# Performance work log

Measured on AMD Instinct MI355X. Metric: run time of the kernel, lower is better.

## Reference

```python
import jax, jax.numpy as jnp
import numpy as np

N_NODES = 50000
N_EDGES = 800000
D = 128


def _graph_conv(x, W, b, src, dst, n_nodes):
    """DGL GraphConv with norm='both': D_in^{-1/2} A D_out^{-1/2} X W + b."""
    ones = jnp.ones((src.shape[0],), dtype=x.dtype)
    out_deg = jax.ops.segment_sum(ones, src, num_segments=n_nodes)
    in_deg = jax.ops.segment_sum(ones, dst, num_segments=n_nodes)
    out_norm = jax.lax.rsqrt(jnp.maximum(out_deg, 1.0))  # [N]
    in_norm = jax.lax.rsqrt(jnp.maximum(in_deg, 1.0))    # [N]
    # scale src features, transform (in_feats == out_feats so order is free), aggregate
    h = (x * out_norm[:, None]) @ W                       # [N, D]
    msgs = h[src]                                         # [E, D] gather
    agg = jax.ops.segment_sum(msgs, dst, num_segments=n_nodes)  # [N, D] scatter-add
    return agg * in_norm[:, None] + b


def setup_inputs() -> dict:
    key = jax.random.key(0)
    ks = jax.random.split(key, 8)
    x = jax.random.normal(ks[0], (N_NODES, D), dtype=jnp.float32)
    src = jax.random.randint(ks[1], (N_EDGES,), 0, N_NODES, dtype=jnp.int64)
    dst = jax.random.randint(ks[2], (N_EDGES,), 0, N_NODES, dtype=jnp.int64)
    scale = 1.0 / np.sqrt(D)
    W1 = jax.random.normal(ks[3], (D, D), dtype=jnp.float32) * scale
    W2 = jax.random.normal(ks[4], (D, D), dtype=jnp.float32) * scale
    W3 = jax.random.normal(ks[5], (D, D), dtype=jnp.float32) * scale
    b1 = jnp.zeros((D,), dtype=jnp.float32)
    b2 = jnp.zeros((D,), dtype=jnp.float32)
    b3 = jnp.zeros((D,), dtype=jnp.float32)
    return {"x": x, "src": src, "dst": dst,
            "W1": W1, "b1": b1, "W2": W2, "b2": b2, "W3": W3, "b3": b3}


def reference(x, src, dst, W1, b1, W2, b2, W3, b3):
    h = _graph_conv(x, W1, b1, src, dst, N_NODES)
    h = jax.nn.relu(h)
    h = _graph_conv(h, W2, b2, src, dst, N_NODES)
    h = jax.nn.relu(h)
    h = _graph_conv(h, W3, b3, src, dst, N_NODES)
    return h
```

## Files before the change

### kernel.cpp

```cpp
#include <hip/hip_runtime.h>
#include <hip/hip_fp16.h>

#define D 128
#define HB 128
#define HT 1024
#define WMAX 12800

struct alignas(16) H8 { __half2 h[4]; };
typedef _Float16 v8h __attribute__((ext_vector_type(8)));
typedef float v4f __attribute__((ext_vector_type(4)));


__global__ __launch_bounds__(HT) void hist_kernel(const int* __restrict__ src,
                                                  const int* __restrict__ dst,
                                                  unsigned* __restrict__ partial_out,
                                                  unsigned* __restrict__ partial_in,
                                                  unsigned char* __restrict__ lrank,
                                                  const float* __restrict__ W1,
                                                  const float* __restrict__ W2,
                                                  const float* __restrict__ W3,
                                                  _Float16* __restrict__ wt,
                                                  int nE, int W, int epb) {
    const int t = threadIdx.x;
    if ((int)blockIdx.x >= 2 * HB) {
        const int l = blockIdx.x - 2 * HB;
        const float* Wsrc = (l == 0) ? W1 : ((l == 1) ? W2 : W3);
        _Float16* o = wt + (size_t)l * D * D;
        for (int i = t; i < D * D; i += HT) {
            const int k = i >> 7, n = i & 127;
            o[n * D + k] = (_Float16)Wsrc[i];
        }
        return;
    }
    __shared__ unsigned lcnt[WMAX];
    const bool is_dst = (blockIdx.x < HB);
    const int b = is_dst ? blockIdx.x : (blockIdx.x - HB);
    for (int i = t; i < W; i += HT) lcnt[i] = 0;
    __syncthreads();
    const int e0 = b * epb;
    const int e1 = min(nE, e0 + epb);
    if (is_dst) {
        for (int e = e0 + t; e < e1; e += HT) {
            const int d = dst[e];
            const unsigned sh = (unsigned)(d & 3) * 8u;
            const unsigned old = atomicAdd(&lcnt[d >> 2], 1u << sh);
            lrank[e] = (unsigned char)((old >> sh) & 0xffu);
        }
    } else {
        for (int e = e0 + t; e < e1; e += HT) {
            const int s = src[e];
            atomicAdd(&lcnt[s >> 2], 1u << ((unsigned)(s & 3) * 8u));
        }
    }
    __syncthreads();
    unsigned* g = (is_dst ? partial_in : partial_out) + (size_t)b * W;
    for (int i = t; i < W; i += HT) g[i] = lcnt[i];
}

__global__ __launch_bounds__(256) void reduce_hist_kernel(const unsigned* __restrict__ partial_out,
                                                          const unsigned* __restrict__ partial_in,
                                                          unsigned* __restrict__ offs_in,
                                                          int* __restrict__ cnt_out,
                                                          int* __restrict__ cnt_in,
                                                          int W, int n, int nbW) {
    const bool is_dst = ((int)blockIdx.x < nbW);
    const int w = (is_dst ? blockIdx.x : (blockIdx.x - nbW)) * 256 + threadIdx.x;
    if (w >= W) return;
    unsigned run = 0;
    if (is_dst) {
#pragma unroll 16
        for (int b = 0; b < HB; ++b) {
            const unsigned c = partial_in[(size_t)b * W + w];
            offs_in[(size_t)b * W + w] = run;
            run += c;
        }
    } else {
#pragma unroll 16
        for (int b = 0; b < HB; ++b) run += partial_out[(size_t)b * W + w];
    }
    int* cnt = is_dst ? cnt_in : cnt_out;
    const int n0 = w * 4;
    const int4 c4 = make_int4((int)(run & 0xffu), (int)((run >> 8) & 0xffu),
                              (int)((run >> 16) & 0xffu), (int)((run >> 24) & 0xffu));
    if (n0 + 3 < n) {
        *(int4*)&cnt[n0] = c4;
    } else {
        const int* cp = &c4.x;
        for (int i = 0; i < 4 && n0 + i < n; ++i) cnt[n0 + i] = cp[i];
    }
}

__global__ __launch_bounds__(1024) void scan_block_kernel(const int* __restrict__ deg,
                                                          int* __restrict__ rp,
                                                          int* __restrict__ bsum, int n) {
    __shared__ int wsum[16];
    const int t = threadIdx.x;
    const int lane = t & 63;
    const int wid = t >> 6;
    const int i = blockIdx.x * 1024 + t;
    const int v = (i < n) ? deg[i] : 0;
    int s = v;
#pragma unroll
    for (int off = 1; off < 64; off <<= 1) {
        int u = __shfl_up(s, off, 64);
        if (lane >= off) s += u;
    }
    if (lane == 63) wsum[wid] = s;
    __syncthreads();
    if (wid == 0) {
        int ws = (lane < 16) ? wsum[lane] : 0;
#pragma unroll
        for (int off = 1; off < 16; off <<= 1) {
            int u = __shfl_up(ws, off, 64);
            if (lane >= off) ws += u;
        }
        if (lane < 16) wsum[lane] = ws;
    }
    __syncthreads();
    const int excl = s - v + ((wid > 0) ? wsum[wid - 1] : 0);
    if (i < n) rp[i] = excl;
    if (t == 0) bsum[blockIdx.x] = wsum[15];
}

__global__ __launch_bounds__(1024) void finalize_kernel(int* __restrict__ rp,
                                                        const int* __restrict__ bsum,
                                                        const int* __restrict__ cnt_out,
                                                        const int* __restrict__ cnt_in,
                                                        float* __restrict__ onorm,
                                                        float* __restrict__ inorm,
                                                        int n, int nb, int nE) {
    __shared__ int prefix_s;
    const int t = threadIdx.x;
    if (t < 64) {
        int v = (t < nb && t < (int)blockIdx.x) ? bsum[t] : 0;
#pragma unroll
        for (int off = 1; off < 64; off <<= 1) v += __shfl_xor(v, off, 64);
        if (t == 0) prefix_s = v;
    }
    __syncthreads();
    const int i = blockIdx.x * 1024 + t;
    if (i < n) {
        rp[i] += prefix_s;
        onorm[i] = rsqrtf(fmaxf((float)cnt_out[i], 1.0f));
        inorm[i] = rsqrtf(fmaxf((float)cnt_in[i], 1.0f));
    }
    if (blockIdx.x == 0 && t == 0) rp[n] = nE;
}

__global__ __launch_bounds__(1024) void gemm1_fill_kernel(
    const float* __restrict__ x, const _Float16* __restrict__ wt,
    const float* __restrict__ onorm, __half* __restrict__ y1, int nrows,
    const int* __restrict__ src, const int* __restrict__ dst,
    const unsigned char* __restrict__ lrank, const unsigned* __restrict__ offs_in,
    const int* __restrict__ rp, int* __restrict__ srcs_sorted,
    int nE, int epb, int W, int nGemmBlocks) {
    __shared__ _Float16 sA[128 * 136];
    __shared__ _Float16 sB[128 * 136];
    const int t = threadIdx.x;

    if ((int)blockIdx.x >= nGemmBlocks) {
        const int e = (blockIdx.x - nGemmBlocks) * 1024 + t;
        if (e < nE) {
            const int d = dst[e];
            const int b = e / epb;
            const unsigned off =
                (offs_in[(size_t)b * W + (d >> 2)] >> ((unsigned)(d & 3) * 8u)) & 0xffu;
            srcs_sorted[rp[d] + (int)off + (int)lrank[e]] = src[e];
        }
        return;
    }

    const int row0 = blockIdx.x * 128;
    const int rr = t >> 4;
    const int c8 = t & 15;
#pragma unroll
    for (int pass = 0; pass < 2; ++pass) {
        const int row = pass * 64 + rr;
        *(float4*)&sB[row * 136 + c8 * 8] = *(const float4*)&wt[(size_t)row * D + c8 * 8];
        const int grow = row0 + row;
        float4 u0 = make_float4(0.f, 0.f, 0.f, 0.f);
        float4 u1 = u0;
        if (grow < nrows) {
            const float* ap = x + (size_t)grow * D + c8 * 8;
            u0 = ((const float4*)ap)[0];
            u1 = ((const float4*)ap)[1];
        }
        v8h hv;
        hv[0] = (_Float16)u0.x; hv[1] = (_Float16)u0.y;
        hv[2] = (_Float16)u0.z; hv[3] = (_Float16)u0.w;
        hv[4] = (_Float16)u1.x; hv[5] = (_Float16)u1.y;
        hv[6] = (_Float16)u1.z; hv[7] = (_Float16)u1.w;
        *(v8h*)&sA[row * 136 + c8 * 8] = hv;
    }
    __syncthreads();

    const int w = t >> 6;
    const int lane = t & 63;
    const int m16 = lane & 15;
    const int quad = lane >> 4;
    const int rt = w >> 1;
    const int ch = w & 1;

    v4f c[4];
#pragma unroll
    for (int ct = 0; ct < 4; ++ct) c[ct] = (v4f){0.f, 0.f, 0.f, 0.f};

#pragma unroll
    for (int ks = 0; ks < 4; ++ks) {
        const v8h a = *(const v8h*)&sA[(rt * 16 + m16) * 136 + ks * 32 + quad * 8];
#pragma unroll
        for (int ct = 0; ct < 4; ++ct) {
            const v8h b = *(const v8h*)&sB[((ch * 4 + ct) * 16 + m16) * 136 + ks * 32 + quad * 8];
            c[ct] = __builtin_amdgcn_mfma_f32_16x16x32_f16(a, b, c[ct], 0, 0, 0);
        }
    }

#pragma unroll
    for (int r = 0; r < 4; ++r) {
        const int row = row0 + rt * 16 + quad * 4 + r;
        if (row < nrows) {
            const float osc = onorm[row];
#pragma unroll
            for (int ct = 0; ct < 4; ++ct) {
                const int col = (ch * 4 + ct) * 16 + m16;
                y1[(size_t)row * D + col] = __float2half(c[ct][r] * osc);
            }
        }
    }
}

template <bool EPI>
__global__ __launch_bounds__(256) void aggregate_kernel(const __half* __restrict__ xh,
                                                        const float* __restrict__ onorm,
                                                        const float* __restrict__ inorm,
                                                        const float* __restrict__ bias,
                                                        const int* __restrict__ rp,
                                                        const int* __restrict__ srcs,
                                                        __half* __restrict__ agg, int n_nodes) {
    const int node = blockIdx.x * 4 + (threadIdx.x >> 6);
    const int lane = threadIdx.x & 63;
    const int rg = lane >> 4;
    const int c8 = lane & 15;
    if (node >= n_nodes) return;
    const int e0 = rp[node];
    const int e1 = rp[node + 1];
    int e = e0 + rg;

    float acc[8];
#pragma unroll
    for (int j = 0; j < 8; ++j) acc[j] = 0.f;

    bool pr[8];
#pragma unroll
    for (int k = 0; k < 8; ++k) pr[k] = (e + 4 * k) < e1;
    int s[8];
#pragma unroll
    for (int k = 0; k < 8; ++k) {
        s[k] = 0;
        if (pr[k]) s[k] = __builtin_nontemporal_load(srcs + e + 4 * k);
    }
    H8 v[8];
#pragma unroll
    for (int k = 0; k < 8; ++k)
        v[k] = ((const H8*)(xh + (size_t)s[k] * D))[c8];
#pragma unroll
    for (int k = 0; k < 8; ++k) {
        if (pr[k]) {
#pragma unroll
            for (int j = 0; j < 4; ++j) {
                acc[2 * j]     = fmaf(__low2float(v[k].h[j]),  1.0f, acc[2 * j]);
                acc[2 * j + 1] = fmaf(__high2float(v[k].h[j]), 1.0f, acc[2 * j + 1]);
            }
        }
    }
    e += 32;

    while (__any(e < e1)) {
        bool q[4];
        int u[4];
#pragma unroll
        for (int k = 0; k < 4; ++k) {
            q[k] = (e + 4 * k) < e1;
            u[k] = 0;
            if (q[k]) u[k] = __builtin_nontemporal_load(srcs + e + 4 * k);
        }
        H8 w[4];
#pragma unroll
        for (int k = 0; k < 4; ++k)
            w[k] = ((const H8*)(xh + (size_t)u[k] * D))[c8];
#pragma unroll
        for (int k = 0; k < 4; ++k) {
            if (q[k]) {
#pragma unroll
                for (int j = 0; j < 4; ++j) {
                    acc[2 * j]     = fmaf(__low2float(w[k].h[j]),  1.0f, acc[2 * j]);
                    acc[2 * j + 1] = fmaf(__high2float(w[k].h[j]), 1.0f, acc[2 * j + 1]);
                }
            }
        }
        e += 16;
    }

    float r[8];
#pragma unroll
    for (int j = 0; j < 8; ++j) r[j] = acc[j];
#pragma unroll
    for (int off = 16; off < 64; off <<= 1)
#pragma unroll
        for (int j = 0; j < 8; ++j) r[j] += __shfl_xor(r[j], off, 64);

    if (rg == 0) {
        if (EPI) {
            const float inm = inorm[node];
            const float onm = onorm[node];
            const float4 bv0 = ((const float4*)bias)[c8 * 2];
            const float4 bv1 = ((const float4*)bias)[c8 * 2 + 1];
            const float* bp0 = &bv0.x;
            const float* bp1 = &bv1.x;
#pragma unroll
            for (int j = 0; j < 4; ++j) {
                r[j]     = fmaxf(fmaf(r[j],     inm, bp0[j]), 0.f) * onm;
                r[j + 4] = fmaxf(fmaf(r[j + 4], inm, bp1[j]), 0.f) * onm;
            }
        }
        H8 h;
#pragma unroll
        for (int j = 0; j < 4; ++j) h.h[j] = __floats2half2_rn(r[2 * j], r[2 * j + 1]);
        ((H8*)(agg + (size_t)node * D))[c8] = h;
    }
}

template <bool FULL, bool RELU, bool OSCALE, bool OUT16>
__global__ __launch_bounds__(256) void gemm_mfma_kernel(const __half* __restrict__ Ah,
                                                        const _Float16* __restrict__ Wt,
                                                        const float* __restrict__ bias,
                                                        const float* __restrict__ inorm,
                                                        const float* __restrict__ onorm,
                                                        void* __restrict__ outv, int nrows) {
    __shared__ _Float16 sA[128 * 136];
    __shared__ _Float16 sB[128 * 136];
    const int t = threadIdx.x;
    const int row0 = blockIdx.x * 128;
    const int rr = t >> 4;
    const int c8 = t & 15;

#pragma unroll
    for (int pass = 0; pass < 8; ++pass) {
        const int row = pass * 16 + rr;
        *(float4*)&sB[row * 136 + c8 * 8] = *(const float4*)&Wt[(size_t)row * D + c8 * 8];
        const int grow = row0 + row;
        float4 v = make_float4(0.f, 0.f, 0.f, 0.f);
        if (grow < nrows)
            v = *(const float4*)((const _Float16*)Ah + (size_t)grow * D + c8 * 8);
        *(float4*)&sA[row * 136 + c8 * 8] = v;
    }
    __syncthreads();

    const int w = t >> 6;
    const int lane = t & 63;
    const int m16 = lane & 15;
    const int quad = lane >> 4;

    v4f c[2][8];
#pragma unroll
    for (int rt = 0; rt < 2; ++rt)
#pragma unroll
        for (int ct = 0; ct < 8; ++ct) c[rt][ct] = (v4f){0.f, 0.f, 0.f, 0.f};

#pragma unroll
    for (int ks = 0; ks < 4; ++ks) {
        v8h afr[2], bfr[8];
#pragma unroll
        for (int rt = 0; rt < 2; ++rt)
            afr[rt] = *(const v8h*)&sA[(w * 32 + rt * 16 + m16) * 136 + ks * 32 + quad * 8];
#pragma unroll
        for (int ct = 0; ct < 8; ++ct)
            bfr[ct] = *(const v8h*)&sB[(ct * 16 + m16) * 136 + ks * 32 + quad * 8];
#pragma unroll
        for (int rt = 0; rt < 2; ++rt)
#pragma unroll
            for (int ct = 0; ct < 8; ++ct)
                c[rt][ct] = __builtin_amdgcn_mfma_f32_16x16x32_f16(afr[rt], bfr[ct], c[rt][ct], 0, 0, 0);
    }

#pragma unroll
    for (int rt = 0; rt < 2; ++rt) {
#pragma unroll
        for (int r = 0; r < 4; ++r) {
            const int row = row0 + w * 32 + rt * 16 + quad * 4 + r;
            if (row < nrows) {
                const float inm = FULL ? inorm[row] : 1.0f;
                const float osc = OSCALE ? onorm[row] : 1.0f;
#pragma unroll
                for (int ct = 0; ct < 8; ++ct) {
                    const int col = ct * 16 + m16;
                    float v = c[rt][ct][r];
                    if (FULL) v = fmaf(v, inm, bias[col]);
                    if (RELU) v = fmaxf(v, 0.f);
                    if (OSCALE) v *= osc;
                    if (OUT16) ((__half*)outv)[(size_t)row * D + col] = __float2half(v);
                    else       ((float*)outv)[(size_t)row * D + col] = v;
                }
            }
        }
    }
}

extern "C" void kernel_launch(void* const* d_in, const int* in_sizes, int n_in,
                              void* d_out, int out_size, void* d_ws, size_t ws_size,
                              hipStream_t stream) {
    const float* x   = (const float*)d_in[0];
    const int*   src = (const int*)d_in[1];
    const int*   dst = (const int*)d_in[2];
    const float* W1  = (const float*)d_in[3];
    const float* b1  = (const float*)d_in[4];
    const float* W2  = (const float*)d_in[5];
    const float* b2  = (const float*)d_in[6];
    const float* W3  = (const float*)d_in[7];
    const float* b3  = (const float*)d_in[8];

    const int N = in_sizes[0] / D;
    const int E = in_sizes[1];

    char* p = (char*)d_ws;
    auto alloc = [&](size_t bytes) -> void* {
        void* r = (void*)p;
        p += (bytes + 255) & ~(size_t)255;
        return r;
    };
    int*           cnt_out = (int*)alloc((size_t)N * 4);
    int*           cnt_in  = (int*)alloc((size_t)N * 4);
    int*           rp      = (int*)alloc((size_t)(N + 1) * 4);
    int*           bsum    = (int*)alloc(1024 * 4);
    float*         onorm   = (float*)alloc((size_t)N * 4);
    float*         inorm   = (float*)alloc((size_t)N * 4);
    int*           srcs    = (int*)alloc((size_t)E * 4);
    unsigned char* lrank   = (unsigned char*)alloc((size_t)E);
    _Float16*      wt      = (_Float16*)alloc((size_t)3 * D * D * 2);
    __half*        hbuf0   = (__half*)alloc((size_t)N * D * 2);
    __half*        hbuf1   = (__half*)alloc((size_t)N * D * 2);
    char*          scratch = (char*)alloc((size_t)3 * HB * ((N + 3) / 4) * 4);

    const int W = (N + 3) / 4;
    const int epb = (E + HB - 1) / HB;
    unsigned* partial_in  = (unsigned*)scratch;
    unsigned* partial_out = partial_in + (size_t)HB * W;
    unsigned* offs_in     = partial_out + (size_t)HB * W;
    __half*   abuf        = (__half*)scratch;
    float*    outf        = (float*)d_out;

    const int nb = (N + 1023) / 1024;
    const int nbW = (W + 255) / 256;
    const int gemmGrid = (N + 127) / 128;
    const int fillGrid = (E + 1023) / 1024;
    const int aggGrid = (N + 3) / 4;

    hist_kernel<<<2 * HB + 3, HT, 0, stream>>>(src, dst, partial_out, partial_in, lrank,
                                               W1, W2, W3, wt, E, W, epb);
    reduce_hist_kernel<<<2 * nbW, 256, 0, stream>>>(partial_out, partial_in, offs_in,
                                                    cnt_out, cnt_in, W, N, nbW);
    scan_block_kernel<<<nb, 1024, 0, stream>>>(cnt_in, rp, bsum, N);
    finalize_kernel<<<nb, 1024, 0, stream>>>(rp, bsum, cnt_out, cnt_in, onorm, inorm, N, nb, E);

    gemm1_fill_kernel<<<gemmGrid + fillGrid, 1024, 0, stream>>>(
        x, wt, onorm, hbuf0, N,
        src, dst, lrank, offs_in, rp, srcs, E, epb, W, gemmGrid);

    aggregate_kernel<true><<<aggGrid, 256, 0, stream>>>(
        hbuf0, onorm, inorm, b1, rp, srcs, hbuf1, N);
    aggregate_kernel<false><<<aggGrid, 256, 0, stream>>>(
        hbuf1, onorm, inorm, b2, rp, srcs, abuf, N);
    gemm_mfma_kernel<true, true, true, true><<<gemmGrid, 256, 0, stream>>>(
        abuf, wt + (size_t)D * D, b2, inorm, onorm, hbuf0, N);
    aggregate_kernel<false><<<aggGrid, 256, 0, stream>>>(
        hbuf0, onorm, inorm, b3, rp, srcs, abuf, N);
    gemm_mfma_kernel<true, false, false, false><<<gemmGrid, 256, 0, stream>>>(
        abuf, wt + (size_t)2 * D * D, b3, inorm, onorm, outf, N);
}
```

Before: 239.3 us.

## Fuse preprocessing kernels and move layer-one out-degree norm into per-edge weights

Merges the histogram, weight-transpose and first GEMM into one launch. The first GEMM no longer needs the out-degree norm, which is instead stored as a per-edge weight during the CSR fill and applied in the first aggregation. The scan is folded into the histogram reduction, and finalize is merged with the fill. The goal is fewer kernel launches and a shorter serial dependency chain before the first aggregation, at the cost of an extra per-edge float array read in the first aggregate and an uncoalesced W1 transpose load inside each GEMM block.

New measurement: 264.1 us. +10.4%, slower.

```diff
diff --git a/kernel.cpp b/kernel.cpp
--- a/kernel.cpp
+++ b/kernel.cpp
@@ -11,7 +11,7 @@
 typedef float v4f __attribute__((ext_vector_type(4)));
 
 
-__global__ __launch_bounds__(HT) void hist_kernel(const int* __restrict__ src,
+__global__ __launch_bounds__(HT) void mega_kernel(const int* __restrict__ src,
                                                   const int* __restrict__ dst,
                                                   unsigned* __restrict__ partial_out,
                                                   unsigned* __restrict__ partial_in,
@@ -20,11 +20,42 @@
                                                   const float* __restrict__ W2,
                                                   const float* __restrict__ W3,
                                                   _Float16* __restrict__ wt,
-                                                  int nE, int W, int epb) {
+                                                  const float* __restrict__ x,
+                                                  __half* __restrict__ y1,
+                                                  int nE, int W, int epb, int nrows) {
+    extern __shared__ char smem[];
     const int t = threadIdx.x;
-    if ((int)blockIdx.x >= 2 * HB) {
-        const int l = blockIdx.x - 2 * HB;
-        const float* Wsrc = (l == 0) ? W1 : ((l == 1) ? W2 : W3);
+
+    if ((int)blockIdx.x < 2 * HB) {
+        unsigned* lcnt = (unsigned*)smem;
+        const bool is_dst = (blockIdx.x < HB);
+        const int b = is_dst ? blockIdx.x : (blockIdx.x - HB);
+        for (int i = t; i < W; i += HT) lcnt[i] = 0;
+        __syncthreads();
+        const int e0 = b * epb;
+        const int e1 = min(nE, e0 + epb);
+        if (is_dst) {
+            for (int e = e0 + t; e < e1; e += HT) {
+                const int d = dst[e];
+                const unsigned sh = (unsigned)(d & 3) * 8u;
+                const unsigned old = atomicAdd(&lcnt[d >> 2], 1u << sh);
+                lrank[e] = (unsigned char)((old >> sh) & 0xffu);
+            }
+        } else {
+            for (int e = e0 + t; e < e1; e += HT) {
+                const int s = src[e];
+                atomicAdd(&lcnt[s >> 2], 1u << ((unsigned)(s & 3) * 8u));
+            }
+        }
+        __syncthreads();
+        unsigned* g = (is_dst ? partial_in : partial_out) + (size_t)b * W;
+        for (int i = t; i < W; i += HT) g[i] = lcnt[i];
+        return;
+    }
+
+    if ((int)blockIdx.x < 2 * HB + 2) {
+        const int l = blockIdx.x - 2 * HB + 1;
+        const float* Wsrc = (l == 1) ? W2 : W3;
         _Float16* o = wt + (size_t)l * D * D;
         for (int i = t; i < D * D; i += HT) {
             const int k = i >> 7, n = i & 127;
@@ -32,151 +63,19 @@
         }
         return;
     }
-    __shared__ unsigned lcnt[WMAX];
-    const bool is_dst = (blockIdx.x < HB);
-    const int b = is_dst ? blockIdx.x : (blockIdx.x - HB);
-    for (int i = t; i < W; i += HT) lcnt[i] = 0;
-    __syncthreads();
-    const int e0 = b * epb;
-    const int e1 = min(nE, e0 + epb);
-    if (is_dst) {
-        for (int e = e0 + t; e < e1; e += HT) {
-            const int d = dst[e];
-            const unsigned sh = (unsigned)(d & 3) * 8u;
-            const unsigned old = atomicAdd(&lcnt[d >> 2], 1u << sh);
-            lrank[e] = (unsigned char)((old >> sh) & 0xffu);
-        }
-    } else {
-        for (int e = e0 + t; e < e1; e += HT) {
-            const int s = src[e];
-            atomicAdd(&lcnt[s >> 2], 1u << ((unsigned)(s & 3) * 8u));
-        }
-    }
-    __syncthreads();
-    unsigned* g = (is_dst ? partial_in : partial_out) + (size_t)b * W;
-    for (int i = t; i < W; i += HT) g[i] = lcnt[i];
-}
-
-__global__ __launch_bounds__(256) void reduce_hist_kernel(const unsigned* __restrict__ partial_out,
-                                                          const unsigned* __restrict__ partial_in,
-                                                          unsigned* __restrict__ offs_in,
-                                                          int* __restrict__ cnt_out,
-                                                          int* __restrict__ cnt_in,
-                                                          int W, int n, int nbW) {
-    const bool is_dst = ((int)blockIdx.x < nbW);
-    const int w = (is_dst ? blockIdx.x : (blockIdx.x - nbW)) * 256 + threadIdx.x;
-    if (w >= W) return;
-    unsigned run = 0;
-    if (is_dst) {
-#pragma unroll 16
-        for (int b = 0; b < HB; ++b) {
-            const unsigned c = partial_in[(size_t)b * W + w];
-            offs_in[(size_t)b * W + w] = run;
-            run += c;
-        }
-    } else {
-#pragma unroll 16
-        for (int b = 0; b < HB; ++b) run += partial_out[(size_t)b * W + w];
-    }
-    int* cnt = is_dst ? cnt_in : cnt_out;
-    const int n0 = w * 4;
-    const int4 c4 = make_int4((int)(run & 0xffu), (int)((run >> 8) & 0xffu),
-                              (int)((run >> 16) & 0xffu), (int)((run >> 24) & 0xffu));
-    if (n0 + 3 < n) {
-        *(int4*)&cnt[n0] = c4;
-    } else {
-        const int* cp = &c4.x;
-        for (int i = 0; i < 4 && n0 + i < n; ++i) cnt[n0 + i] = cp[i];
-    }
-}
-
-__global__ __launch_bounds__(1024) void scan_block_kernel(const int* __restrict__ deg,
-                                                          int* __restrict__ rp,
-                                                          int* __restrict__ bsum, int n) {
-    __shared__ int wsum[16];
-    const int t = threadIdx.x;
-    const int lane = t & 63;
-    const int wid = t >> 6;
-    const int i = blockIdx.x * 1024 + t;
-    const int v = (i < n) ? deg[i] : 0;
-    int s = v;
-#pragma unroll
-    for (int off = 1; off < 64; off <<= 1) {
-        int u = __shfl_up(s, off, 64);
-        if (lane >= off) s += u;
-    }
-    if (lane == 63) wsum[wid] = s;
-    __syncthreads();
-    if (wid == 0) {
-        int ws = (lane < 16) ? wsum[lane] : 0;
-#pragma unroll
-        for (int off = 1; off < 16; off <<= 1) {
-            int u = __shfl_up(ws, off, 64);
-            if (lane >= off) ws += u;
-        }
-        if (lane < 16) wsum[lane] = ws;
-    }
-    __syncthreads();
-    const int excl = s - v + ((wid > 0) ? wsum[wid - 1] : 0);
-    if (i < n) rp[i] = excl;
-    if (t == 0) bsum[blockIdx.x] = wsum[15];
-}
-
-__global__ __launch_bounds__(1024) void finalize_kernel(int* __restrict__ rp,
-                                                        const int* __restrict__ bsum,
-                                                        const int* __restrict__ cnt_out,
-                                                        const int* __restrict__ cnt_in,
-                                                        float* __restrict__ onorm,
-                                                        float* __restrict__ inorm,
-                                                        int n, int nb, int nE) {
-    __shared__ int prefix_s;
-    const int t = threadIdx.x;
-    if (t < 64) {
-        int v = (t < nb && t < (int)blockIdx.x) ? bsum[t] : 0;
-#pragma unroll
-        for (int off = 1; off < 64; off <<= 1) v += __shfl_xor(v, off, 64);
-        if (t == 0) prefix_s = v;
-    }
-    __syncthreads();
-    const int i = blockIdx.x * 1024 + t;
-    if (i < n) {
-        rp[i] += prefix_s;
-        onorm[i] = rsqrtf(fmaxf((float)cnt_out[i], 1.0f));
-        inorm[i] = rsqrtf(fmaxf((float)cnt_in[i], 1.0f));
-    }
-    if (blockIdx.x == 0 && t == 0) rp[n] = nE;
-}
-
-__global__ __launch_bounds__(1024) void gemm1_fill_kernel(
-    const float* __restrict__ x, const _Float16* __restrict__ wt,
-    const float* __restrict__ onorm, __half* __restrict__ y1, int nrows,
-    const int* __restrict__ src, const int* __restrict__ dst,
-    const unsigned char* __restrict__ lrank, const unsigned* __restrict__ offs_in,
-    const int* __restrict__ rp, int* __restrict__ srcs_sorted,
-    int nE, int epb, int W, int nGemmBlocks) {
-    __shared__ _Float16 sA[128 * 136];
-    __shared__ _Float16 sB[128 * 136];
-    const int t = threadIdx.x;
-
-    if ((int)blockIdx.x >= nGemmBlocks) {
-        const int e = (blockIdx.x - nGemmBlocks) * 1024 + t;
-        if (e < nE) {
-            const int d = dst[e];
-            const int b = e / epb;
-            const unsigned off =
-                (offs_in[(size_t)b * W + (d >> 2)] >> ((unsigned)(d & 3) * 8u)) & 0xffu;
-            srcs_sorted[rp[d] + (int)off + (int)lrank[e]] = src[e];
-        }
-        return;
-    }
-
-    const int row0 = blockIdx.x * 128;
+
+    _Float16* sA = (_Float16*)smem;
+    _Float16* sB = sA + 128 * 136;
+    const int blk = blockIdx.x - (2 * HB + 2);
+    const int row0 = blk * 128;
     const int rr = t >> 4;
     const int c8 = t & 15;
 #pragma unroll
     for (int pass = 0; pass < 2; ++pass) {
         const int row = pass * 64 + rr;
-        *(float4*)&sB[row * 136 + c8 * 8] = *(const float4*)&wt[(size_t)row * D + c8 * 8];
+#pragma unroll
+        for (int j = 0; j < 8; ++j)
+            sB[row * 136 + c8 * 8 + j] = (_Float16)W1[(size_t)(c8 * 8 + j) * D + row];
         const int grow = row0 + row;
         float4 u0 = make_float4(0.f, 0.f, 0.f, 0.f);
         float4 u1 = u0;
@@ -219,23 +118,168 @@
     for (int r = 0; r < 4; ++r) {
         const int row = row0 + rt * 16 + quad * 4 + r;
         if (row < nrows) {
-            const float osc = onorm[row];
 #pragma unroll
             for (int ct = 0; ct < 4; ++ct) {
                 const int col = (ch * 4 + ct) * 16 + m16;
-                y1[(size_t)row * D + col] = __float2half(c[ct][r] * osc);
+                y1[(size_t)row * D + col] = __float2half(c[ct][r]);
             }
         }
     }
 }
 
-template <bool EPI>
+__global__ __launch_bounds__(256) void reduce_scan_kernel(const unsigned* __restrict__ partial_out,
+                                                          const unsigned* __restrict__ partial_in,
+                                                          unsigned* __restrict__ offs_in,
+                                                          int* __restrict__ cnt_out,
+                                                          int* __restrict__ cnt_in,
+                                                          int* __restrict__ rpp,
+                                                          int* __restrict__ bsum,
+                                                          int W, int n, int nbW) {
+    const int t = threadIdx.x;
+    if ((int)blockIdx.x >= nbW) {
+        const int w = (blockIdx.x - nbW) * 256 + t;
+        if (w >= W) return;
+        unsigned run = 0;
+#pragma unroll 16
+        for (int b = 0; b < HB; ++b) run += partial_out[(size_t)b * W + w];
+        const int n0 = w * 4;
+        const int4 c4 = make_int4((int)(run & 0xffu), (int)((run >> 8) & 0xffu),
+                                  (int)((run >> 16) & 0xffu), (int)((run >> 24) & 0xffu));
+        if (n0 + 3 < n) {
+            *(int4*)&cnt_out[n0] = c4;
+        } else {
+            const int* cp = &c4.x;
+            for (int i = 0; i < 4 && n0 + i < n; ++i) cnt_out[n0 + i] = cp[i];
+        }
+        return;
+    }
+
+    __shared__ int ws[4];
+    const int w = blockIdx.x * 256 + t;
+    unsigned run = 0;
+    if (w < W) {
+#pragma unroll 16
+        for (int b = 0; b < HB; ++b) {
+            const unsigned c = partial_in[(size_t)b * W + w];
+            offs_in[(size_t)b * W + w] = run;
+            run += c;
+        }
+    }
+    const int n0 = w * 4;
+    int c0 = (int)(run & 0xffu), c1 = (int)((run >> 8) & 0xffu);
+    int c2 = (int)((run >> 16) & 0xffu), c3 = (int)((run >> 24) & 0xffu);
+    if (n0 >= n)     { c0 = 0; c1 = 0; c2 = 0; c3 = 0; }
+    else if (n0 + 1 >= n) { c1 = 0; c2 = 0; c3 = 0; }
+    else if (n0 + 2 >= n) { c2 = 0; c3 = 0; }
+    else if (n0 + 3 >= n) { c3 = 0; }
+
+    if (w < W) {
+        const int4 c4 = make_int4(c0, c1, c2, c3);
+        if (n0 + 3 < n) {
+            *(int4*)&cnt_in[n0] = c4;
+        } else {
+            const int* cp = &c4.x;
+            for (int i = 0; i < 4 && n0 + i < n; ++i) cnt_in[n0 + i] = cp[i];
+        }
+    }
+
+    const int lane = t & 63;
+    const int wid = t >> 6;
+    const int T = c0 + c1 + c2 + c3;
+    int sincl = T;
+#pragma unroll
+    for (int off = 1; off < 64; off <<= 1) {
+        int u = __shfl_up(sincl, off, 64);
+        if (lane >= off) sincl += u;
+    }
+    if (lane == 63) ws[wid] = sincl;
+    __syncthreads();
+    int wbase = 0;
+#pragma unroll
+    for (int j = 0; j < 4; ++j) wbase += (j < wid) ? ws[j] : 0;
+    const int excl = wbase + sincl - T;
+
+    if (w < W && n0 < n) {
+        const int4 r4 = make_int4(excl, excl + c0, excl + c0 + c1, excl + c0 + c1 + c2);
+        if (n0 + 3 < n) {
+            *(int4*)&rpp[n0] = r4;
+        } else {
+            const int* rp4 = &r4.x;
+            for (int i = 0; i < 4 && n0 + i < n; ++i) rpp[n0 + i] = rp4[i];
+        }
+    }
+    if (t == 255) bsum[blockIdx.x] = wbase + sincl;
+}
+
+__global__ __launch_bounds__(1024) void finalize_fill_kernel(const int* __restrict__ rpp,
+                                                             const int* __restrict__ bsum,
+                                                             const int* __restrict__ cnt_out,
+                                                             const int* __restrict__ cnt_in,
+                                                             int* __restrict__ rp,
+                                                             float* __restrict__ onorm,
+                                                             float* __restrict__ inorm,
+                                                             const int* __restrict__ src,
+                                                             const int* __restrict__ dst,
+                                                             const unsigned char* __restrict__ lrank,
+                                                             const unsigned* __restrict__ offs_in,
+                                                             int* __restrict__ srcs_sorted,
+                                                             float* __restrict__ wsorted,
+                                                             int n, int nb, int nE, int epb, int W) {
+    const int t = threadIdx.x;
+    if ((int)blockIdx.x < nb) {
+        __shared__ int prefix_s;
+        if (t < 64) {
+            int v = (t < nb && t < (int)blockIdx.x) ? bsum[t] : 0;
+#pragma unroll
+            for (int off = 1; off < 64; off <<= 1) v += __shfl_xor(v, off, 64);
+            if (t == 0) prefix_s = v;
+        }
+        __syncthreads();
+        const int i = blockIdx.x * 1024 + t;
+        if (i < n) {
+            rp[i] = rpp[i] + prefix_s;
+            onorm[i] = rsqrtf(fmaxf((float)cnt_out[i], 1.0f));
+            inorm[i] = rsqrtf(fmaxf((float)cnt_in[i], 1.0f));
+        }
+        if (blockIdx.x == 0 && t == 0) rp[n] = nE;
+        return;
+    }
+
+    __shared__ int bpref[64];
+    if (t < 64) {
+        int v = (t < nb) ? bsum[t] : 0;
+        const int lane = t;
+#pragma unroll
+        for (int off = 1; off < 64; off <<= 1) {
+            int u = __shfl_up(v, off, 64);
+            if (lane >= off) v += u;
+        }
+        bpref[t] = v;
+    }
+    __syncthreads();
+    const int e = (blockIdx.x - nb) * 1024 + t;
+    if (e < nE) {
+        const int d = dst[e];
+        const int b = e / epb;
+        const unsigned off =
+            (offs_in[(size_t)b * W + (d >> 2)] >> ((unsigned)(d & 3) * 8u)) & 0xffu;
+        const int blkd = d >> 10;
+        const int rpf = rpp[d] + (blkd ? bpref[blkd - 1] : 0);
+        const int slot = rpf + (int)off + (int)lrank[e];
+        const int s = src[e];
+        srcs_sorted[slot] = s;
+        wsorted[slot] = rsqrtf(fmaxf((float)cnt_out[s], 1.0f));
+    }
+}
+
+template <bool EPI, bool WEIGHTED>
 __global__ __launch_bounds__(256) void aggregate_kernel(const __half* __restrict__ xh,
                                                         const float* __restrict__ onorm,
                                                         const float* __restrict__ inorm,
                                                         const float* __restrict__ bias,
                                                         const int* __restrict__ rp,
                                                         const int* __restrict__ srcs,
+                                                        const float* __restrict__ wsrt,
                                                         __half* __restrict__ agg, int n_nodes) {
     const int node = blockIdx.x * 4 + (threadIdx.x >> 6);
     const int lane = threadIdx.x & 63;
@@ -254,10 +298,15 @@
 #pragma unroll
     for (int k = 0; k < 8; ++k) pr[k] = (e + 4 * k) < e1;
     int s[8];
+    float wk[8];
 #pragma unroll
     for (int k = 0; k < 8; ++k) {
         s[k] = 0;
         if (pr[k]) s[k] = __builtin_nontemporal_load(srcs + e + 4 * k);
+        if (WEIGHTED) {
+            wk[k] = 0.f;
+            if (pr[k]) wk[k] = __builtin_nontemporal_load(wsrt + e + 4 * k);
+        }
     }
     H8 v[8];
 #pragma unroll
@@ -265,7 +314,13 @@
         v[k] = ((const H8*)(xh + (size_t)s[k] * D))[c8];
 #pragma unroll
     for (int k = 0; k < 8; ++k) {
-        if (pr[k]) {
+        if (WEIGHTED) {
+#pragma unroll
+            for (int j = 0; j < 4; ++j) {
+                acc[2 * j]     = fmaf(__low2float(v[k].h[j]),  wk[k], acc[2 * j]);
+                acc[2 * j + 1] = fmaf(__high2float(v[k].h[j]), wk[k], acc[2 * j + 1]);
+            }
+        } else if (pr[k]) {
 #pragma unroll
             for (int j = 0; j < 4; ++j) {
                 acc[2 * j]     = fmaf(__low2float(v[k].h[j]),  1.0f, acc[2 * j]);
@@ -278,23 +333,34 @@
     while (__any(e < e1)) {
         bool q[4];
         int u[4];
+        float wq[4];
 #pragma unroll
         for (int k = 0; k < 4; ++k) {
             q[k] = (e + 4 * k) < e1;
             u[k] = 0;
             if (q[k]) u[k] = __builtin_nontemporal_load(srcs + e + 4 * k);
-        }
-        H8 w[4];
+            if (WEIGHTED) {
+                wq[k] = 0.f;
+                if (q[k]) wq[k] = __builtin_nontemporal_load(wsrt + e + 4 * k);
+            }
+        }
+        H8 w4[4];
 #pragma unroll
         for (int k = 0; k < 4; ++k)
-            w[k] = ((const H8*)(xh + (size_t)u[k] * D))[c8];
+            w4[k] = ((const H8*)(xh + (size_t)u[k] * D))[c8];
 #pragma unroll
         for (int k = 0; k < 4; ++k) {
-            if (q[k]) {
+            if (WEIGHTED) {
 #pragma unroll
                 for (int j = 0; j < 4; ++j) {
-                    acc[2 * j]     = fmaf(__low2float(w[k].h[j]),  1.0f, acc[2 * j]);
-                    acc[2 * j + 1] = fmaf(__high2float(w[k].h[j]), 1.0f, acc[2 * j + 1]);
+                    acc[2 * j]     = fmaf(__low2float(w4[k].h[j]),  wq[k], acc[2 * j]);
+                    acc[2 * j + 1] = fmaf(__high2float(w4[k].h[j]), wq[k], acc[2 * j + 1]);
+                }
+            } else if (q[k]) {
+#pragma unroll
+                for (int j = 0; j < 4; ++j) {
+                    acc[2 * j]     = fmaf(__low2float(w4[k].h[j]),  1.0f, acc[2 * j]);
+                    acc[2 * j + 1] = fmaf(__high2float(w4[k].h[j]), 1.0f, acc[2 * j + 1]);
                 }
             }
         }
@@ -431,10 +497,12 @@
     int*           cnt_out = (int*)alloc((size_t)N * 4);
     int*           cnt_in  = (int*)alloc((size_t)N * 4);
     int*           rp      = (int*)alloc((size_t)(N + 1) * 4);
+    int*           rpp     = (int*)alloc((size_t)(N + 1) * 4);
     int*           bsum    = (int*)alloc(1024 * 4);
     float*         onorm   = (float*)alloc((size_t)N * 4);
     float*         inorm   = (float*)alloc((size_t)N * 4);
     int*           srcs    = (int*)alloc((size_t)E * 4);
+    float*         wsorted = (float*)alloc((size_t)E * 4);
     unsigned char* lrank   = (unsigned char*)alloc((size_t)E);
     _Float16*      wt      = (_Float16*)alloc((size_t)3 * D * D * 2);
     __half*        hbuf0   = (__half*)alloc((size_t)N * D * 2);
@@ -454,26 +522,25 @@
     const int gemmGrid = (N + 127) / 128;
     const int fillGrid = (E + 1023) / 1024;
     const int aggGrid = (N + 3) / 4;
-
-    hist_kernel<<<2 * HB + 3, HT, 0, stream>>>(src, dst, partial_out, partial_in, lrank,
-                                               W1, W2, W3, wt, E, W, epb);
-    reduce_hist_kernel<<<2 * nbW, 256, 0, stream>>>(partial_out, partial_in, offs_in,
-                                                    cnt_out, cnt_in, W, N, nbW);
-    scan_block_kernel<<<nb, 1024, 0, stream>>>(cnt_in, rp, bsum, N);
-    finalize_kernel<<<nb, 1024, 0, stream>>>(rp, bsum, cnt_out, cnt_in, onorm, inorm, N, nb, E);
-
-    gemm1_fill_kernel<<<gemmGrid + fillGrid, 1024, 0, stream>>>(
-        x, wt, onorm, hbuf0, N,
-        src, dst, lrank, offs_in, rp, srcs, E, epb, W, gemmGrid);
-
-    aggregate_kernel<true><<<aggGrid, 256, 0, stream>>>(
-        hbuf0, onorm, inorm, b1, rp, srcs, hbuf1, N);
-    aggregate_kernel<false><<<aggGrid, 256, 0, stream>>>(
-        hbuf1, onorm, inorm, b2, rp, srcs, abuf, N);
+    const size_t megaLds = (size_t)2 * 128 * 136 * sizeof(_Float16);
+
+    mega_kernel<<<2 * HB + 2 + gemmGrid, HT, megaLds, stream>>>(
+        src, dst, partial_out, partial_in, lrank, W1, W2, W3, wt, x, hbuf0,
+        E, W, epb, N);
+    reduce_scan_kernel<<<2 * nbW, 256, 0, stream>>>(partial_out, partial_in, offs_in,
+                                                    cnt_out, cnt_in, rpp, bsum, W, N, nbW);
+    finalize_fill_kernel<<<nb + fillGrid, 1024, 0, stream>>>(
+        rpp, bsum, cnt_out, cnt_in, rp, onorm, inorm,
+        src, dst, lrank, offs_in, srcs, wsorted, N, nb, E, epb, W);
+
+    aggregate_kernel<true, true><<<aggGrid, 256, 0, stream>>>(
+        hbuf0, onorm, inorm, b1, rp, srcs, wsorted, hbuf1, N);
+    aggregate_kernel<false, false><<<aggGrid, 256, 0, stream>>>(
+        hbuf1, onorm, inorm, b2, rp, srcs, nullptr, abuf, N);
     gemm_mfma_kernel<true, true, true, true><<<gemmGrid, 256, 0, stream>>>(
         abuf, wt + (size_t)D * D, b2, inorm, onorm, hbuf0, N);
-    aggregate_kernel<false><<<aggGrid, 256, 0, stream>>>(
-        hbuf0, onorm, inorm, b3, rp, srcs, abuf, N);
+    aggregate_kernel<false, false><<<aggGrid, 256, 0, stream>>>(
+        hbuf0, onorm, inorm, b3, rp, srcs, nullptr, abuf, N);
     gemm_mfma_kernel<true, false, false, false><<<gemmGrid, 256, 0, stream>>>(
         abuf, wt + (size_t)2 * D * D, b3, inorm, onorm, outf, N);
 }
```

## Fuse the degree scan into the histogram reduce; tune the aggregate kernel

Applied to the files above, without the earlier changes.

The in-degree block scan now runs inside the histogram reduce kernel. Each 256-thread block scans the 1024 node counts it has just reduced and writes partial row pointers plus a block sum, which removes the separate scan_block_kernel launch and its re-read of cnt_in. finalize then adds the block prefix into a new rpp buffer. Separately, the aggregate kernel gets a launch_bounds occupancy hint of 8 and uses 32-bit H8 index arithmetic for its gathers, aiming for cheaper address math and more waves in flight. This adds an extra row-pointer buffer, and the occupancy hint may cost register spills.

Result: slower. 255.7 us (+6.8%).

```diff
diff --git a/kernel.cpp b/kernel.cpp
--- a/kernel.cpp
+++ b/kernel.cpp
@@ -57,75 +57,95 @@
     for (int i = t; i < W; i += HT) g[i] = lcnt[i];
 }
 
-__global__ __launch_bounds__(256) void reduce_hist_kernel(const unsigned* __restrict__ partial_out,
+__global__ __launch_bounds__(256) void reduce_scan_kernel(const unsigned* __restrict__ partial_out,
                                                           const unsigned* __restrict__ partial_in,
                                                           unsigned* __restrict__ offs_in,
                                                           int* __restrict__ cnt_out,
                                                           int* __restrict__ cnt_in,
+                                                          int* __restrict__ rpp,
+                                                          int* __restrict__ bsum,
                                                           int W, int n, int nbW) {
-    const bool is_dst = ((int)blockIdx.x < nbW);
-    const int w = (is_dst ? blockIdx.x : (blockIdx.x - nbW)) * 256 + threadIdx.x;
-    if (w >= W) return;
+    const int t = threadIdx.x;
+    if ((int)blockIdx.x >= nbW) {
+        const int w = (blockIdx.x - nbW) * 256 + t;
+        if (w >= W) return;
+        unsigned run = 0;
+#pragma unroll 16
+        for (int b = 0; b < HB; ++b) run += partial_out[(size_t)b * W + w];
+        const int n0 = w * 4;
+        const int4 c4 = make_int4((int)(run & 0xffu), (int)((run >> 8) & 0xffu),
+                                  (int)((run >> 16) & 0xffu), (int)((run >> 24) & 0xffu));
+        if (n0 + 3 < n) {
+            *(int4*)&cnt_out[n0] = c4;
+        } else {
+            const int* cp = &c4.x;
+            for (int i = 0; i < 4 && n0 + i < n; ++i) cnt_out[n0 + i] = cp[i];
+        }
+        return;
+    }
+
+    __shared__ int ws[4];
+    const int w = blockIdx.x * 256 + t;
     unsigned run = 0;
-    if (is_dst) {
+    if (w < W) {
 #pragma unroll 16
         for (int b = 0; b < HB; ++b) {
             const unsigned c = partial_in[(size_t)b * W + w];
             offs_in[(size_t)b * W + w] = run;
             run += c;
         }
-    } else {
-#pragma unroll 16
-        for (int b = 0; b < HB; ++b) run += partial_out[(size_t)b * W + w];
-    }
-    int* cnt = is_dst ? cnt_in : cnt_out;
+    }
     const int n0 = w * 4;
-    const int4 c4 = make_int4((int)(run & 0xffu), (int)((run >> 8) & 0xffu),
-                              (int)((run >> 16) & 0xffu), (int)((run >> 24) & 0xffu));
-    if (n0 + 3 < n) {
-        *(int4*)&cnt[n0] = c4;
-    } else {
-        const int* cp = &c4.x;
-        for (int i = 0; i < 4 && n0 + i < n; ++i) cnt[n0 + i] = cp[i];
-    }
-}
-
-__global__ __launch_bounds__(1024) void scan_block_kernel(const int* __restrict__ deg,
-                                                          int* __restrict__ rp,
-                                                          int* __restrict__ bsum, int n) {
-    __shared__ int wsum[16];
-    const int t = threadIdx.x;
+    int c0 = (int)(run & 0xffu), c1 = (int)((run >> 8) & 0xffu);
+    int c2 = (int)((run >> 16) & 0xffu), c3 = (int)((run >> 24) & 0xffu);
+    if (n0 >= n)          { c0 = 0; c1 = 0; c2 = 0; c3 = 0; }
+    else if (n0 + 1 >= n) { c1 = 0; c2 = 0; c3 = 0; }
+    else if (n0 + 2 >= n) { c2 = 0; c3 = 0; }
+    else if (n0 + 3 >= n) { c3 = 0; }
+
+    if (w < W) {
+        const int4 c4 = make_int4(c0, c1, c2, c3);
+        if (n0 + 3 < n) {
+            *(int4*)&cnt_in[n0] = c4;
+        } else {
+            const int* cp = &c4.x;
+            for (int i = 0; i < 4 && n0 + i < n; ++i) cnt_in[n0 + i] = cp[i];
+        }
+    }
+
     const int lane = t & 63;
     const int wid = t >> 6;
-    const int i = blockIdx.x * 1024 + t;
-    const int v = (i < n) ? deg[i] : 0;
-    int s = v;
+    const int T = c0 + c1 + c2 + c3;
+    int sincl = T;
 #pragma unroll
     for (int off = 1; off < 64; off <<= 1) {
-        int u = __shfl_up(s, off, 64);
-        if (lane >= off) s += u;
-    }
-    if (lane == 63) wsum[wid] = s;
+        int u = __shfl_up(sincl, off, 64);
+        if (lane >= off) sincl += u;
+    }
+    if (lane == 63) ws[wid] = sincl;
     __syncthreads();
-    if (wid == 0) {
-        int ws = (lane < 16) ? wsum[lane] : 0;
-#pragma unroll
-        for (int off = 1; off < 16; off <<= 1) {
-            int u = __shfl_up(ws, off, 64);
-            if (lane >= off) ws += u;
-        }
-        if (lane < 16) wsum[lane] = ws;
-    }
-    __syncthreads();
-    const int excl = s - v + ((wid > 0) ? wsum[wid - 1] : 0);
-    if (i < n) rp[i] = excl;
-    if (t == 0) bsum[blockIdx.x] = wsum[15];
-}
-
-__global__ __launch_bounds__(1024) void finalize_kernel(int* __restrict__ rp,
+    int wbase = 0;
+#pragma unroll
+    for (int j = 0; j < 4; ++j) wbase += (j < wid) ? ws[j] : 0;
+    const int excl = wbase + sincl - T;
+
+    if (w < W && n0 < n) {
+        const int4 r4 = make_int4(excl, excl + c0, excl + c0 + c1, excl + c0 + c1 + c2);
+        if (n0 + 3 < n) {
+            *(int4*)&rpp[n0] = r4;
+        } else {
+            const int* rp4 = &r4.x;
+            for (int i = 0; i < 4 && n0 + i < n; ++i) rpp[n0 + i] = rp4[i];
+        }
+    }
+    if (t == 255) bsum[blockIdx.x] = wbase + sincl;
+}
+
+__global__ __launch_bounds__(1024) void finalize_kernel(const int* __restrict__ rpp,
                                                         const int* __restrict__ bsum,
                                                         const int* __restrict__ cnt_out,
                                                         const int* __restrict__ cnt_in,
+                                                        int* __restrict__ rp,
                                                         float* __restrict__ onorm,
                                                         float* __restrict__ inorm,
                                                         int n, int nb, int nE) {
@@ -140,7 +160,7 @@
     __syncthreads();
     const int i = blockIdx.x * 1024 + t;
     if (i < n) {
-        rp[i] += prefix_s;
+        rp[i] = rpp[i] + prefix_s;
         onorm[i] = rsqrtf(fmaxf((float)cnt_out[i], 1.0f));
         inorm[i] = rsqrtf(fmaxf((float)cnt_in[i], 1.0f));
     }
@@ -230,13 +250,13 @@
 }
 
 template <bool EPI>
-__global__ __launch_bounds__(256) void aggregate_kernel(const __half* __restrict__ xh,
-                                                        const float* __restrict__ onorm,
-                                                        const float* __restrict__ inorm,
-                                                        const float* __restrict__ bias,
-                                                        const int* __restrict__ rp,
-                                                        const int* __restrict__ srcs,
-                                                        __half* __restrict__ agg, int n_nodes) {
+__global__ __launch_bounds__(256, 8) void aggregate_kernel(const __half* __restrict__ xh,
+                                                           const float* __restrict__ onorm,
+                                                           const float* __restrict__ inorm,
+                                                           const float* __restrict__ bias,
+                                                           const int* __restrict__ rp,
+                                                           const int* __restrict__ srcs,
+                                                           __half* __restrict__ agg, int n_nodes) {
     const int node = blockIdx.x * 4 + (threadIdx.x >> 6);
     const int lane = threadIdx.x & 63;
     const int rg = lane >> 4;
@@ -245,6 +265,7 @@
     const int e0 = rp[node];
     const int e1 = rp[node + 1];
     int e = e0 + rg;
+    const H8* xh8 = (const H8*)xh;
 
     float acc[8];
 #pragma unroll
@@ -262,7 +283,7 @@
     H8 v[8];
 #pragma unroll
     for (int k = 0; k < 8; ++k)
-        v[k] = ((const H8*)(xh + (size_t)s[k] * D))[c8];
+        v[k] = xh8[(unsigned)(s[k] * 16 + c8)];
 #pragma unroll
     for (int k = 0; k < 8; ++k) {
         if (pr[k]) {
@@ -287,7 +308,7 @@
         H8 w[4];
 #pragma unroll
         for (int k = 0; k < 4; ++k)
-            w[k] = ((const H8*)(xh + (size_t)u[k] * D))[c8];
+            w[k] = xh8[(unsigned)(u[k] * 16 + c8)];
 #pragma unroll
         for (int k = 0; k < 4; ++k) {
             if (q[k]) {
@@ -431,6 +452,7 @@
     int*           cnt_out = (int*)alloc((size_t)N * 4);
     int*           cnt_in  = (int*)alloc((size_t)N * 4);
     int*           rp      = (int*)alloc((size_t)(N + 1) * 4);
+    int*           rpp     = (int*)alloc((size_t)(N + 1) * 4);
     int*           bsum    = (int*)alloc(1024 * 4);
     float*         onorm   = (float*)alloc((size_t)N * 4);
     float*         inorm   = (float*)alloc((size_t)N * 4);
@@ -457,11 +479,10 @@
 
     hist_kernel<<<2 * HB + 3, HT, 0, stream>>>(src, dst, partial_out, partial_in, lrank,
                                                W1, W2, W3, wt, E, W, epb);
-    reduce_hist_kernel<<<2 * nbW, 256, 0, stream>>>(partial_out, partial_in, offs_in,
-                                                    cnt_out, cnt_in, W, N, nbW);
-    scan_block_kernel<<<nb, 1024, 0, stream>>>(cnt_in, rp, bsum, N);
-    finalize_kernel<<<nb, 1024, 0, stream>>>(rp, bsum, cnt_out, cnt_in, onorm, inorm, N, nb, E);
-
+    reduce_scan_kernel<<<2 * nbW, 256, 0, stream>>>(partial_out, partial_in, offs_in,
+                                                    cnt_out, cnt_in, rpp, bsum, W, N, nbW);
+    finalize_kernel<<<nb, 1024, 0, stream>>>(rpp, bsum, cnt_out, cnt_in, rp,
+                                             onorm, inorm, N, nb, E);
     gemm1_fill_kernel<<<gemmGrid + fillGrid, 1024, 0, stream>>>(
         x, wt, onorm, hbuf0, N,
         src, dst, lrank, offs_in, rp, srcs, E, epb, W, gemmGrid);
```
